# Performance work log

Hardware: AMD Instinct MI355X
Metric: run time of the kernel (lower is better)

## Reference

```python
import jax, jax.numpy as jnp
import numpy as np

N_NODES = 100000
N_EDGES = 1600000
IN_DIM = 128
HID = 128
OUT_DIM = 64
EPS = 1e-8


def setup_inputs() -> dict:
    key = jax.random.key(0)
    ks = jax.random.split(key, 10)
    x = jax.random.normal(ks[0], (N_NODES, IN_DIM), dtype=jnp.float32)
    edge_index = jax.random.randint(ks[1], (2, N_EDGES), 0, N_NODES, dtype=jnp.int64)
    edge_attr = jax.random.uniform(ks[2], (N_EDGES, 4), dtype=jnp.float32)
    s1 = 1.0 / np.sqrt(IN_DIM)
    s2 = 1.0 / np.sqrt(HID)
    sr = 1.0 / np.sqrt(2 * HID)
    W1 = jax.random.normal(ks[3], (HID, IN_DIM), dtype=jnp.float32) * s1
    b1 = jnp.zeros((HID,), dtype=jnp.float32)
    W2 = jax.random.normal(ks[4], (HID, HID), dtype=jnp.float32) * s2
    b2 = jnp.zeros((HID,), dtype=jnp.float32)
    Wr = jax.random.normal(ks[5], (OUT_DIM, 2 * HID), dtype=jnp.float32) * sr
    br = jnp.zeros((OUT_DIM,), dtype=jnp.float32)
    return {"x": x, "edge_index": edge_index, "edge_attr": edge_attr,
            "W1": W1, "b1": b1, "W2": W2, "b2": b2, "Wr": Wr, "br": br}


def _edge_weight_from_attr_auto(edge_attr):
    # mean over features, min-max normalize, invert, clamp >= 0
    m = edge_attr.mean(axis=-1)                      # [E]
    m_min, m_max = m.min(), m.max()
    m_norm = (m - m_min) / (m_max - m_min + EPS)
    w = jnp.where(m_max - m_min > EPS, 1.0 - m_norm, jnp.ones_like(m))
    return jnp.clip(w, 0.0)


def reference(x, edge_index, edge_attr, W1, b1, W2, b2, Wr, br):
    N = x.shape[0]
    row, col = edge_index[0], edge_index[1]          # source -> target
    ew = _edge_weight_from_attr_auto(edge_attr)      # [E]
    # GCN normalization with self-loops (self-loop weight = 1.0)
    deg = jax.ops.segment_sum(ew, col, num_segments=N) + 1.0   # [N]
    dis = jax.lax.rsqrt(deg)                         # deg >= 1
    norm = dis[row] * ew * dis[col]                  # [E]

    def gcn(h, W, b):
        hW = h @ W.T                                 # [N, d_out]
        agg = jax.ops.segment_sum(norm[:, None] * hW[row], col, num_segments=N)
        # self-loop contribution: dis[i] * 1.0 * dis[i] * hW[i]
        return agg + (dis * dis)[:, None] * hW + b

    # dropout in eval mode -> identity
    h1 = jax.nn.relu(gcn(x, W1, b1))                 # [N, HID]
    h2 = jax.nn.relu(gcn(h1, W2, b2))                # [N, HID]
    hcat = jnp.concatenate([h1, h2], axis=-1)        # [N, 2*HID] (JK concat)
    return hcat @ Wr.T + br                          # residue-level [N, OUT_DIM]
```

## Files before the change

### kernel.cpp

```cpp
#include <hip/hip_runtime.h>

#define NN 100000
#define NE 1600000
#define HID 128
#define ODIM 64
#define NBK 196
#define BSHIFT 9
#define BGRID 800
#define CVTB 48
#define CHUNK 2000
#define BITER 8
#define BINCAP 12288
#define SMAX 2588
#define LMAX 647

typedef unsigned int u32;
typedef unsigned short u16;
typedef __bf16 bf16x8 __attribute__((ext_vector_type(8)));
typedef float f32x4 __attribute__((ext_vector_type(4)));
typedef float f32x2 __attribute__((ext_vector_type(2)));

__device__ __forceinline__ float bf_lo(u32 p){ return __uint_as_float(p << 16); }
__device__ __forceinline__ float bf_hi(u32 p){ return __uint_as_float(p & 0xffff0000u); }
__device__ __forceinline__ u16 f2bf(float f){
  u32 u = __float_as_uint(f);
  u += 0x7fffu + ((u >> 16) & 1u);
  return (u16)(u >> 16);
}
__device__ __forceinline__ bf16x8 ld8bf(const u16* p){ return *(const bf16x8*)p; }
__device__ __forceinline__ bf16x8 cvt8(const float* p){
  union { bf16x8 v; u16 s[8]; } r;
#pragma unroll
  for (int i = 0; i < 8; i++) r.s[i] = f2bf(p[i]);
  return r.v;
}

__device__ __forceinline__ void wparams(const u32* minmax, float* A, float* B){
  u32 mnq = 32767u - minmax[0];
  u32 mxq = minmax[1];
  u32 rngq = mxq - mnq;
  float inv = rngq ? 1.f / ((float)rngq * (1.f / 32767.f) + 1e-8f) : 0.f;
  *A = 1.f + (float)mnq * (1.f / 32767.f) * inv;
  *B = inv * (1.f / 32767.f);
}

__global__ __launch_bounds__(256) void k_bin(
    const float* __restrict__ eattr, const int* __restrict__ erow,
    const int* __restrict__ ecol, u32* __restrict__ bcur,
    u32* __restrict__ binA, u16* __restrict__ binM, u32* __restrict__ minmax,
    const float* __restrict__ W1, const float* __restrict__ W2,
    const float* __restrict__ Wr, u16* __restrict__ W1b,
    u16* __restrict__ W2b, u16* __restrict__ Wrb){
  int tid = threadIdx.x;
  if (blockIdx.x >= BGRID){
    int i = (blockIdx.x - BGRID) * 256 + tid;
    const float* src; u16* dst; int off;
    if (i < 4096){ src = W1; dst = W1b; off = i; }
    else if (i < 8192){ src = W2; dst = W2b; off = i - 4096; }
    else { src = Wr; dst = Wrb; off = i - 8192; }
    float4 v = ((const float4*)src)[off];
    uint2 o;
    o.x = (u32)f2bf(v.x) | ((u32)f2bf(v.y) << 16);
    o.y = (u32)f2bf(v.z) | ((u32)f2bf(v.w) << 16);
    ((uint2*)dst)[off] = o;
    return;
  }
  __shared__ u32 lcnt4[4 * NBK], wof4[4 * NBK];
  __shared__ u32 lofs[NBK], gb[NBK];
  __shared__ u32 scn[256];
  __shared__ u16 lmap[LMAX];
  __shared__ u32 stageA[SMAX];
  __shared__ u16 stageM[SMAX];
  __shared__ u32 Tt;
  __shared__ u32 sMn[4], sMx[4];
  for (int t = tid; t < 4 * NBK; t += 256) lcnt4[t] = 0;
  __syncthreads();
  int base = blockIdx.x * CHUNK;
  int wid = tid >> 6, lane = tid & 63;
  u32 lmn = 0, lmx = 0;
  u32 pk[BITER], sd[BITER], mq8[BITER];
#pragma unroll
  for (int it = 0; it < BITER; it++){
    int idx = it * 256 + tid;
    u32 p = 0xFFFFFFFFu, srcd = 0, mq = 0;
    if (idx < CHUNK){
      int e = base + idx;
      float4 a = ((const float4*)eattr)[e];
      float m = 0.25f * (a.x + a.y + a.z + a.w);
      mq = (u32)(m * 32767.f + 0.5f);
      lmn = max(lmn, 32767u - mq); lmx = max(lmx, mq);
      int c = ecol[e];
      u32 s = (u32)erow[e]; if (s >= NN) s = 0;
      if ((u32)c < NN){
        u32 b = (u32)c >> BSHIFT;
        u32 r = atomicAdd(&lcnt4[wid * NBK + b], 1u);
        p = (b << 21) | r;
        srcd = s | (((u32)c & 511u) << 17);
      }
    }
    pk[it] = p; sd[it] = srcd; mq8[it] = mq;
  }
  __syncthreads();
  u32 na = 0, n = 0;
  if (tid < NBK){
    u32 n0 = lcnt4[tid], n1 = lcnt4[NBK + tid];
    u32 n2 = lcnt4[2 * NBK + tid], n3 = lcnt4[3 * NBK + tid];
    n = n0 + n1 + n2 + n3;
    na = (n + 3u) & ~3u;
    wof4[tid] = 0; wof4[NBK + tid] = n0;
    wof4[2 * NBK + tid] = n0 + n1; wof4[3 * NBK + tid] = n0 + n1 + n2;
  }
  scn[tid] = na; __syncthreads();
  for (int s = 1; s < 256; s <<= 1){
    u32 t = (tid >= s) ? scn[tid - s] : 0;
    __syncthreads();
    scn[tid] += t;
    __syncthreads();
  }
  u32 ex = scn[tid] - na;
  if (tid < NBK){
    lofs[tid] = ex;
    u32 g = 0x80000000u;
    if (na){
      u32 gl = atomicAdd(&bcur[tid], na);
      if (gl + na <= BINCAP) g = (u32)tid * BINCAP + gl;
    }
    gb[tid] = g;
    for (u32 l = ex >> 2; l < (ex + na) >> 2; l++) lmap[l] = (u16)tid;
    for (u32 k = n; k < na; k++){ stageA[ex + k] = 0xFFFFFFFFu; stageM[ex + k] = 0; }
  }
  if (tid == 255) Tt = scn[255];
  __syncthreads();
#pragma unroll
  for (int it = 0; it < BITER; it++){
    u32 p = pk[it];
    if (p == 0xFFFFFFFFu) continue;
    u32 b = p >> 21;
    u32 slot = lofs[b] + wof4[wid * NBK + b] + (p & 4095u);
    stageA[slot] = sd[it];
    stageM[slot] = (u16)mq8[it];
  }
  __syncthreads();
  u32 T = Tt;
  for (u32 i = tid; i < T; i += 256){
    u32 b = lmap[i >> 2];
    u32 g = gb[b];
    if (g != 0x80000000u){
      u32 o = g + (i - lofs[b]);
      binA[o] = stageA[i];
      binM[o] = stageM[i];
    }
  }
  for (int off = 32; off; off >>= 1){
    lmn = max(lmn, (u32)__shfl_xor((int)lmn, off));
    lmx = max(lmx, (u32)__shfl_xor((int)lmx, off));
  }
  if (lane == 0){ sMn[wid] = lmn; sMx[wid] = lmx; }
  __syncthreads();
  if (tid == 0){
    u32 mn = max(max(sMn[0], sMn[1]), max(sMn[2], sMn[3]));
    u32 mx = max(max(sMx[0], sMx[1]), max(sMx[2], sMx[3]));
    atomicMax(&minmax[0], mn);
    atomicMax(&minmax[1], mx);
  }
}

__global__ __launch_bounds__(1024) void k_scatter(
    const u32* __restrict__ bcur, const u32* __restrict__ binA,
    const u16* __restrict__ binM, const u32* __restrict__ minmax,
    u32* __restrict__ csr, u32* __restrict__ meta, float* __restrict__ dis){
  __shared__ u32 cntL[512], sumL[512], curL[512];
  __shared__ u32 wtot[8];
  int b = blockIdx.x, tid = threadIdx.x;
  int bb = b * BINCAP;
  int nrec = (int)min(bcur[b], (u32)BINCAP);
  if (tid < 512){ cntL[tid] = 0; sumL[tid] = 0; }
  __syncthreads();
  for (int i = tid; i < nrec; i += 1024){
    u32 a = binA[bb + i];
    if (a == 0xFFFFFFFFu) continue;
    u32 d = (a >> 17) & 511u;
    u32 mq = binM[bb + i];
    atomicAdd(&cntL[d], 1u);
    atomicAdd(&sumL[d], mq);
  }
  __syncthreads();
  float A, B; wparams(minmax, &A, &B);
  int wid = tid >> 6, lane = tid & 63;
  u32 v = 0, incl = 0;
  if (tid < 512){ v = cntL[tid]; incl = v; }
  for (int off = 1; off < 64; off <<= 1){
    u32 t = (u32)__shfl_up((int)incl, off);
    if (lane >= off) incl += t;
  }
  if (tid < 512 && lane == 63) wtot[wid] = incl;
  __syncthreads();
  if (tid < 512){
    u32 pre = 0;
#pragma unroll
    for (int k = 0; k < 8; k++) pre += (k < wid) ? wtot[k] : 0u;
    u32 ex = pre + incl - v;
    curL[tid] = (u32)bb + ex;
    int node = (b << BSHIFT) + tid;
    if (node < NN){
      meta[node] = ((u32)bb + ex) | (v << 22);
      float sw = A * (float)v - B * (float)sumL[tid];
      dis[node] = rsqrtf(1.f + sw);
    }
  }
  __syncthreads();
  for (int i = tid; i < nrec; i += 1024){
    u32 a = binA[bb + i];
    if (a == 0xFFFFFFFFu) continue;
    u32 d = (a >> 17) & 511u;
    u32 mq = binM[bb + i];
    u32 pos = atomicAdd(&curL[d], 1u);
    csr[pos] = (a & 0x1FFFFu) | (mq << 17);
  }
}

template <bool A_F32>
__global__ __launch_bounds__(256) void k_gemm128(
    const void* __restrict__ Av, const u16* __restrict__ Bt,
    const float* __restrict__ dis, u16* __restrict__ G){
  int wave = threadIdx.x >> 6, lane = threadIdx.x & 63;
  int m0 = blockIdx.x * 32;
  int m = lane & 15, q = lane >> 4;
  const float* a0f = (const float*)Av + (size_t)(m0 + m) * HID;
  const float* a1f = a0f + (size_t)16 * HID;
  const u16*   a0b = (const u16*)Av   + (size_t)(m0 + m) * HID;
  const u16*   a1b = a0b + (size_t)16 * HID;
  const u16* brow0 = Bt + (size_t)(wave * 16 + m) * HID;
  const u16* brow1 = brow0 + (size_t)64 * HID;
  f32x4 acc00 = {0.f,0.f,0.f,0.f}, acc01 = {0.f,0.f,0.f,0.f};
  f32x4 acc10 = {0.f,0.f,0.f,0.f}, acc11 = {0.f,0.f,0.f,0.f};
#pragma unroll
  for (int kb = 0; kb < HID; kb += 32){
    bf16x8 af0 = A_F32 ? cvt8(a0f + kb + q * 8) : ld8bf(a0b + kb + q * 8);
    bf16x8 af1 = A_F32 ? cvt8(a1f + kb + q * 8) : ld8bf(a1b + kb + q * 8);
    bf16x8 bf0 = ld8bf(brow0 + kb + q * 8);
    bf16x8 bf1 = ld8bf(brow1 + kb + q * 8);
    acc00 = __builtin_amdgcn_mfma_f32_16x16x32_bf16(af0, bf0, acc00, 0, 0, 0);
    acc01 = __builtin_amdgcn_mfma_f32_16x16x32_bf16(af0, bf1, acc01, 0, 0, 0);
    acc10 = __builtin_amdgcn_mfma_f32_16x16x32_bf16(af1, bf0, acc10, 0, 0, 0);
    acc11 = __builtin_amdgcn_mfma_f32_16x16x32_bf16(af1, bf1, acc11, 0, 0, 0);
  }
  u16* crow0 = G + (size_t)(m0 + q * 4) * HID + wave * 16 + m;
  u16* crow1 = crow0 + (size_t)16 * HID;
#pragma unroll
  for (int r = 0; r < 4; r++){
    float d0 = dis[m0 + q * 4 + r];
    float d1 = dis[m0 + 16 + q * 4 + r];
    crow0[(size_t)r * HID]      = f2bf(acc00[r] * d0);
    crow0[(size_t)r * HID + 64] = f2bf(acc01[r] * d0);
    crow1[(size_t)r * HID]      = f2bf(acc10[r] * d1);
    crow1[(size_t)r * HID + 64] = f2bf(acc11[r] * d1);
  }
}

__global__ __launch_bounds__(256) void k_aggregate(
    const u32* __restrict__ meta, const u32* __restrict__ csr,
    const float* __restrict__ dis, const u32* __restrict__ minmax,
    const u16* __restrict__ g, const float* __restrict__ bias,
    u16* __restrict__ hout){
  int node = __builtin_amdgcn_readfirstlane(
      (int)(blockIdx.x * 4 + (threadIdx.x >> 6)));
  int lane = threadIdx.x & 63;
  const u32* gp = (const u32*)g;
  u32 sv = gp[((size_t)node << 6) + lane];
  u32 mw = meta[node];
  float di = dis[node];
  float A, B; wparams(minmax, &A, &B);
  u32 s = mw & 0x3FFFFFu;
  int c = (int)(mw >> 22);
  const u32* cp = csr + s;
  f32x2 acc = {0.f, 0.f};
  int j = 0;
  for (; j + 16 <= c; j += 16){
    u32 p[16];
#pragma unroll
    for (int t = 0; t < 16; t++)
      p[t] = __builtin_amdgcn_readfirstlane(cp[j + t]);
    u32 pv[16];
#pragma unroll
    for (int t = 0; t < 16; t++)
      pv[t] = gp[(size_t)(p[t] & 0x1FFFFu) * 64u + lane];
#pragma unroll
    for (int t = 0; t < 16; t++){
      float wf = A - B * (float)(p[t] >> 17);
      f32x2 val = {bf_lo(pv[t]), bf_hi(pv[t])};
      f32x2 w2 = {wf, wf};
      acc += w2 * val;
    }
  }
  for (; j < c; j += 8){
    u32 p[8];
#pragma unroll
    for (int t = 0; t < 8; t++)
      p[t] = __builtin_amdgcn_readfirstlane(cp[j + t]);
    u32 st[8]; float wv[8];
#pragma unroll
    for (int t = 0; t < 8; t++){
      bool ok = (j + t) < c;
      st[t] = ok ? (p[t] & 0x1FFFFu) : 0u;
      wv[t] = ok ? (A - B * (float)(p[t] >> 17)) : 0.f;
    }
    u32 pv[8];
#pragma unroll
    for (int t = 0; t < 8; t++)
      pv[t] = gp[(size_t)st[t] * 64u + lane];
#pragma unroll
    for (int t = 0; t < 8; t++){
      f32x2 val = {bf_lo(pv[t]), bf_hi(pv[t])};
      f32x2 w2 = {wv[t], wv[t]};
      acc += w2 * val;
    }
  }
  float2 bv = ((const float2*)bias)[lane];
  f32x2 selfv = {bf_lo(sv), bf_hi(sv)};
  float o0 = fmaxf((acc.x + selfv.x) * di + bv.x, 0.f);
  float o1 = fmaxf((acc.y + selfv.y) * di + bv.y, 0.f);
  ((u32*)hout)[((size_t)node << 6) + lane] = (u32)f2bf(o0) | ((u32)f2bf(o1) << 16);
}

__global__ __launch_bounds__(256) void k_readout(
    const u16* __restrict__ h1, const u16* __restrict__ h2,
    const u16* __restrict__ Wrb, const float* __restrict__ br, float* __restrict__ out){
  int wave = threadIdx.x >> 6, lane = threadIdx.x & 63;
  int m0 = blockIdx.x * 32;
  int n0 = wave * 16;
  int m = lane & 15, q = lane >> 4;
  const u16* a10 = h1 + (size_t)(m0 + m) * HID;
  const u16* a11 = a10 + (size_t)16 * HID;
  const u16* a20 = h2 + (size_t)(m0 + m) * HID;
  const u16* a21 = a20 + (size_t)16 * HID;
  const u16* b  = Wrb + (size_t)(n0 + m) * (2 * HID);
  f32x4 acc0 = {0.f,0.f,0.f,0.f}, acc1 = {0.f,0.f,0.f,0.f};
#pragma unroll
  for (int kb = 0; kb < HID; kb += 32){
    bf16x8 bf = ld8bf(b + kb + q * 8);
    acc0 = __builtin_amdgcn_mfma_f32_16x16x32_bf16(ld8bf(a10 + kb + q * 8), bf, acc0, 0, 0, 0);
    acc1 = __builtin_amdgcn_mfma_f32_16x16x32_bf16(ld8bf(a11 + kb + q * 8), bf, acc1, 0, 0, 0);
  }
#pragma unroll
  for (int kb = 0; kb < HID; kb += 32){
    bf16x8 bf = ld8bf(b + HID + kb + q * 8);
    acc0 = __builtin_amdgcn_mfma_f32_16x16x32_bf16(ld8bf(a20 + kb + q * 8), bf, acc0, 0, 0, 0);
    acc1 = __builtin_amdgcn_mfma_f32_16x16x32_bf16(ld8bf(a21 + kb + q * 8), bf, acc1, 0, 0, 0);
  }
  float bias = br[n0 + m];
  float* crow0 = out + (size_t)(m0 + q * 4) * ODIM + n0 + m;
  float* crow1 = crow0 + (size_t)16 * ODIM;
#pragma unroll
  for (int r = 0; r < 4; r++){
    crow0[(size_t)r * ODIM] = acc0[r] + bias;
    crow1[(size_t)r * ODIM] = acc1[r] + bias;
  }
}

extern "C" void kernel_launch(void* const* d_in, const int* in_sizes, int n_in,
                              void* d_out, int out_size, void* d_ws, size_t ws_size,
                              hipStream_t stream){
  const float* x     = (const float*)d_in[0];
  const int*   eidx  = (const int*)d_in[1];
  const float* eattr = (const float*)d_in[2];
  const float* W1    = (const float*)d_in[3];
  const float* b1    = (const float*)d_in[4];
  const float* W2    = (const float*)d_in[5];
  const float* b2    = (const float*)d_in[6];
  const float* Wr    = (const float*)d_in[7];
  const float* br    = (const float*)d_in[8];
  const int* erow  = eidx;
  const int* ecol  = eidx + NE;

  char* w = (char*)d_ws;
  auto carve = [&](size_t bytes) -> void* {
    void* p = (void*)w;
    w += (bytes + 255) & ~(size_t)255;
    return p;
  };
  u32* csr       = (u32*)carve((size_t)NBK * BINCAP * 4);
  u32* bcur      = (u32*)carve(1024);
  u32* minmax    = (u32*)carve(256);
  u32* meta      = (u32*)carve((size_t)NN * 4);
  float* dis     = (float*)carve((size_t)NN * 4);
  u16* W1b       = (u16*)carve((size_t)HID * HID * 2);
  u16* W2b       = (u16*)carve((size_t)HID * HID * 2);
  u16* Wrb       = (u16*)carve((size_t)ODIM * 2 * HID * 2);
  u16* g         = (u16*)carve((size_t)NN * HID * 2);
  u16* h1        = (u16*)carve((size_t)NN * HID * 2);
  u16* h2        = (u16*)carve((size_t)NN * HID * 2);
  u32* binA      = (u32*)h2;
  u16* binM      = (u16*)((char*)h2 + (size_t)NBK * BINCAP * 4);

  hipMemsetAsync(bcur, 0, 1280, stream);
  k_bin<<<BGRID + CVTB, 256, 0, stream>>>(eattr, erow, ecol, bcur, binA, binM,
                                          minmax, W1, W2, Wr, W1b, W2b, Wrb);
  k_scatter<<<NBK, 1024, 0, stream>>>(bcur, binA, binM, minmax, csr, meta, dis);

  k_gemm128<true><<<NN / 32, 256, 0, stream>>>(x, W1b, dis, g);
  k_aggregate<<<NN / 4, 256, 0, stream>>>(meta, csr, dis, minmax, g, b1, h1);
  k_gemm128<false><<<NN / 32, 256, 0, stream>>>(h1, W2b, dis, g);
  k_aggregate<<<NN / 4, 256, 0, stream>>>(meta, csr, dis, minmax, g, b2, h2);
  k_readout<<<NN / 32, 256, 0, stream>>>(h1, h2, Wrb, br, (float*)d_out);
}
```

Baseline: 397.4 us.

## Fuse first-layer GEMM into edge-binning kernel and apply source dis during aggregation

The layer-1 x@W1 GEMM now runs as extra blocks of the front binning kernel, so it can overlap with edge binning instead of waiting for dis. Because dis is not yet known there, the raw product is stored and the first aggregation multiplies each edge weight by dis[src] with a gather, scaling the self term by dis[i]. This removes one kernel launch and the W1 conversion step, at the cost of an extra scattered dis load per edge in layer-1 aggregation and W1 being converted from fp32 inside every GEMM block. The launch-bounds occupancy hint and the conversion block count also change.

Measured after the change: 390.5 us. Within noise of the previous version (-1.7%).

```diff
diff --git a/kernel.cpp b/kernel.cpp
--- a/kernel.cpp
+++ b/kernel.cpp
@@ -7,7 +7,8 @@
 #define NBK 196
 #define BSHIFT 9
 #define BGRID 800
-#define CVTB 48
+#define CVTB 32
+#define GEMMB 3125
 #define CHUNK 2000
 #define BITER 8
 #define BINCAP 12288
@@ -44,20 +45,53 @@
   *B = inv * (1.f / 32767.f);
 }
 
-__global__ __launch_bounds__(256) void k_bin(
+__global__ __launch_bounds__(256, 4) void k_front(
     const float* __restrict__ eattr, const int* __restrict__ erow,
     const int* __restrict__ ecol, u32* __restrict__ bcur,
     u32* __restrict__ binA, u16* __restrict__ binM, u32* __restrict__ minmax,
-    const float* __restrict__ W1, const float* __restrict__ W2,
-    const float* __restrict__ Wr, u16* __restrict__ W1b,
-    u16* __restrict__ W2b, u16* __restrict__ Wrb){
+    const float* __restrict__ x, const float* __restrict__ W1,
+    const float* __restrict__ W2, const float* __restrict__ Wr,
+    u16* __restrict__ W2b, u16* __restrict__ Wrb, u16* __restrict__ graw){
   int tid = threadIdx.x;
-  if (blockIdx.x >= BGRID){
-    int i = (blockIdx.x - BGRID) * 256 + tid;
+  int bid = blockIdx.x;
+  if (bid >= BGRID + CVTB){
+    int gblk = bid - BGRID - CVTB;
+    int wave = tid >> 6, lane = tid & 63;
+    int m0 = gblk * 32;
+    int m = lane & 15, q = lane >> 4;
+    const float* a0f = x + (size_t)(m0 + m) * HID;
+    const float* a1f = a0f + (size_t)16 * HID;
+    const float* brow0 = W1 + (size_t)(wave * 16 + m) * HID;
+    const float* brow1 = brow0 + (size_t)64 * HID;
+    f32x4 acc00 = {0.f,0.f,0.f,0.f}, acc01 = {0.f,0.f,0.f,0.f};
+    f32x4 acc10 = {0.f,0.f,0.f,0.f}, acc11 = {0.f,0.f,0.f,0.f};
+#pragma unroll
+    for (int kb = 0; kb < HID; kb += 32){
+      bf16x8 af0 = cvt8(a0f + kb + q * 8);
+      bf16x8 af1 = cvt8(a1f + kb + q * 8);
+      bf16x8 bf0 = cvt8(brow0 + kb + q * 8);
+      bf16x8 bf1 = cvt8(brow1 + kb + q * 8);
+      acc00 = __builtin_amdgcn_mfma_f32_16x16x32_bf16(af0, bf0, acc00, 0, 0, 0);
+      acc01 = __builtin_amdgcn_mfma_f32_16x16x32_bf16(af0, bf1, acc01, 0, 0, 0);
+      acc10 = __builtin_amdgcn_mfma_f32_16x16x32_bf16(af1, bf0, acc10, 0, 0, 0);
+      acc11 = __builtin_amdgcn_mfma_f32_16x16x32_bf16(af1, bf1, acc11, 0, 0, 0);
+    }
+    u16* crow0 = graw + (size_t)(m0 + q * 4) * HID + wave * 16 + m;
+    u16* crow1 = crow0 + (size_t)16 * HID;
+#pragma unroll
+    for (int r = 0; r < 4; r++){
+      crow0[(size_t)r * HID]      = f2bf(acc00[r]);
+      crow0[(size_t)r * HID + 64] = f2bf(acc01[r]);
+      crow1[(size_t)r * HID]      = f2bf(acc10[r]);
+      crow1[(size_t)r * HID + 64] = f2bf(acc11[r]);
+    }
+    return;
+  }
+  if (bid >= BGRID){
+    int i = (bid - BGRID) * 256 + tid;
     const float* src; u16* dst; int off;
-    if (i < 4096){ src = W1; dst = W1b; off = i; }
-    else if (i < 8192){ src = W2; dst = W2b; off = i - 4096; }
-    else { src = Wr; dst = Wrb; off = i - 8192; }
+    if (i < 4096){ src = W2; dst = W2b; off = i; }
+    else { src = Wr; dst = Wrb; off = i - 4096; }
     float4 v = ((const float4*)src)[off];
     uint2 o;
     o.x = (u32)f2bf(v.x) | ((u32)f2bf(v.y) << 16);
@@ -75,7 +109,7 @@
   __shared__ u32 sMn[4], sMx[4];
   for (int t = tid; t < 4 * NBK; t += 256) lcnt4[t] = 0;
   __syncthreads();
-  int base = blockIdx.x * CHUNK;
+  int base = bid * CHUNK;
   int wid = tid >> 6, lane = tid & 63;
   u32 lmn = 0, lmx = 0;
   u32 pk[BITER], sd[BITER], mq8[BITER];
@@ -219,25 +253,22 @@
   }
 }
 
-template <bool A_F32>
 __global__ __launch_bounds__(256) void k_gemm128(
-    const void* __restrict__ Av, const u16* __restrict__ Bt,
+    const u16* __restrict__ Ab, const u16* __restrict__ Bt,
     const float* __restrict__ dis, u16* __restrict__ G){
   int wave = threadIdx.x >> 6, lane = threadIdx.x & 63;
   int m0 = blockIdx.x * 32;
   int m = lane & 15, q = lane >> 4;
-  const float* a0f = (const float*)Av + (size_t)(m0 + m) * HID;
-  const float* a1f = a0f + (size_t)16 * HID;
-  const u16*   a0b = (const u16*)Av   + (size_t)(m0 + m) * HID;
-  const u16*   a1b = a0b + (size_t)16 * HID;
+  const u16* a0b = Ab + (size_t)(m0 + m) * HID;
+  const u16* a1b = a0b + (size_t)16 * HID;
   const u16* brow0 = Bt + (size_t)(wave * 16 + m) * HID;
   const u16* brow1 = brow0 + (size_t)64 * HID;
   f32x4 acc00 = {0.f,0.f,0.f,0.f}, acc01 = {0.f,0.f,0.f,0.f};
   f32x4 acc10 = {0.f,0.f,0.f,0.f}, acc11 = {0.f,0.f,0.f,0.f};
 #pragma unroll
   for (int kb = 0; kb < HID; kb += 32){
-    bf16x8 af0 = A_F32 ? cvt8(a0f + kb + q * 8) : ld8bf(a0b + kb + q * 8);
-    bf16x8 af1 = A_F32 ? cvt8(a1f + kb + q * 8) : ld8bf(a1b + kb + q * 8);
+    bf16x8 af0 = ld8bf(a0b + kb + q * 8);
+    bf16x8 af1 = ld8bf(a1b + kb + q * 8);
     bf16x8 bf0 = ld8bf(brow0 + kb + q * 8);
     bf16x8 bf1 = ld8bf(brow1 + kb + q * 8);
     acc00 = __builtin_amdgcn_mfma_f32_16x16x32_bf16(af0, bf0, acc00, 0, 0, 0);
@@ -258,6 +289,7 @@
   }
 }
 
+template <bool FD>
 __global__ __launch_bounds__(256) void k_aggregate(
     const u32* __restrict__ meta, const u32* __restrict__ csr,
     const float* __restrict__ dis, const u32* __restrict__ minmax,
@@ -288,6 +320,7 @@
 #pragma unroll
     for (int t = 0; t < 16; t++){
       float wf = A - B * (float)(p[t] >> 17);
+      if (FD) wf *= dis[p[t] & 0x1FFFFu];
       f32x2 val = {bf_lo(pv[t]), bf_hi(pv[t])};
       f32x2 w2 = {wf, wf};
       acc += w2 * val;
@@ -303,7 +336,9 @@
     for (int t = 0; t < 8; t++){
       bool ok = (j + t) < c;
       st[t] = ok ? (p[t] & 0x1FFFFu) : 0u;
-      wv[t] = ok ? (A - B * (float)(p[t] >> 17)) : 0.f;
+      float wf = A - B * (float)(p[t] >> 17);
+      if (FD) wf *= dis[st[t]];
+      wv[t] = ok ? wf : 0.f;
     }
     u32 pv[8];
 #pragma unroll
@@ -318,8 +353,9 @@
   }
   float2 bv = ((const float2*)bias)[lane];
   f32x2 selfv = {bf_lo(sv), bf_hi(sv)};
-  float o0 = fmaxf((acc.x + selfv.x) * di + bv.x, 0.f);
-  float o1 = fmaxf((acc.y + selfv.y) * di + bv.y, 0.f);
+  float sc = FD ? di : 1.f;
+  float o0 = fmaxf((acc.x + sc * selfv.x) * di + bv.x, 0.f);
+  float o1 = fmaxf((acc.y + sc * selfv.y) * di + bv.y, 0.f);
   ((u32*)hout)[((size_t)node << 6) + lane] = (u32)f2bf(o0) | ((u32)f2bf(o1) << 16);
 }
 
@@ -384,7 +420,6 @@
   u32* minmax    = (u32*)carve(256);
   u32* meta      = (u32*)carve((size_t)NN * 4);
   float* dis     = (float*)carve((size_t)NN * 4);
-  u16* W1b       = (u16*)carve((size_t)HID * HID * 2);
   u16* W2b       = (u16*)carve((size_t)HID * HID * 2);
   u16* Wrb       = (u16*)carve((size_t)ODIM * 2 * HID * 2);
   u16* g         = (u16*)carve((size_t)NN * HID * 2);
@@ -394,13 +429,12 @@
   u16* binM      = (u16*)((char*)h2 + (size_t)NBK * BINCAP * 4);
 
   hipMemsetAsync(bcur, 0, 1280, stream);
-  k_bin<<<BGRID + CVTB, 256, 0, stream>>>(eattr, erow, ecol, bcur, binA, binM,
-                                          minmax, W1, W2, Wr, W1b, W2b, Wrb);
+  k_front<<<BGRID + CVTB + GEMMB, 256, 0, stream>>>(
+      eattr, erow, ecol, bcur, binA, binM, minmax,
+      x, W1, W2, Wr, W2b, Wrb, g);
   k_scatter<<<NBK, 1024, 0, stream>>>(bcur, binA, binM, minmax, csr, meta, dis);
-
-  k_gemm128<true><<<NN / 32, 256, 0, stream>>>(x, W1b, dis, g);
-  k_aggregate<<<NN / 4, 256, 0, stream>>>(meta, csr, dis, minmax, g, b1, h1);
-  k_gemm128<false><<<NN / 32, 256, 0, stream>>>(h1, W2b, dis, g);
-  k_aggregate<<<NN / 4, 256, 0, stream>>>(meta, csr, dis, minmax, g, b2, h2);
+  k_aggregate<true><<<NN / 4, 256, 0, stream>>>(meta, csr, dis, minmax, g, b1, h1);
+  k_gemm128<<<NN / 32, 256, 0, stream>>>(h1, W2b, dis, g);
+  k_aggregate<false><<<NN / 4, 256, 0, stream>>>(meta, csr, dis, minmax, g, b2, h2);
   k_readout<<<NN / 32, 256, 0, stream>>>(h1, h2, Wrb, br, (float*)d_out);
 }
```
